# Kernel tuning notes

Measured on AMD Instinct MI355X. Metric: run time of the kernel, lower is better.

## Reference

```python
import jax, jax.numpy as jnp
import numpy as np
from jax import lax

L, H = 16384, 1024
EPS = 1e-5


def _ln(x, w, b):
    m = jnp.mean(x, axis=-1, keepdims=True)
    v = jnp.var(x, axis=-1, keepdims=True)
    return (x - m) * lax.rsqrt(v + EPS) * w + b


def setup_inputs() -> dict:
    key = jax.random.key(0)
    ks = jax.random.split(key, 12)
    s = 0.02
    return {
        "x": jax.random.normal(ks[0], (L, H), dtype=jnp.float32),
        "ln1_w": jnp.ones((H,), jnp.float32),
        "ln1_b": jnp.zeros((H,), jnp.float32),
        "W_in": jax.random.normal(ks[1], (H, H), jnp.float32) * s,
        "b_in": jnp.zeros((H,), jnp.float32),
        "W_gate": jax.random.normal(ks[2], (H, H), jnp.float32) * s,
        "b_gate": jnp.zeros((H,), jnp.float32),
        "W_out": jax.random.normal(ks[3], (H, H), jnp.float32) * s,
        "b_out": jnp.zeros((H,), jnp.float32),
        "state_decay": jnp.zeros((H,), jnp.float32),
        "ln2_w": jnp.ones((H,), jnp.float32),
        "ln2_b": jnp.zeros((H,), jnp.float32),
        "W_ff1": jax.random.normal(ks[4], (H, 2 * H), jnp.float32) * s,
        "b_ff1": jnp.zeros((2 * H,), jnp.float32),
        "W_ff2": jax.random.normal(ks[5], (2 * H, H), jnp.float32) * s,
        "b_ff2": jnp.zeros((H,), jnp.float32),
    }


def reference(x, ln1_w, ln1_b, W_in, b_in, W_gate, b_gate, W_out, b_out,
              state_decay, ln2_w, ln2_b, W_ff1, b_ff1, W_ff2, b_ff2):
    hidden = _ln(x, ln1_w, ln1_b)                       # [L,H]
    u = hidden @ W_in + b_in                            # [L,H]
    gate = jax.nn.sigmoid(hidden @ W_gate + b_gate)     # [L,H]
    decay = jax.nn.sigmoid(state_decay)                 # [H]

    def step(s, u_t):
        s = decay * s + u_t
        return s, s

    z = jnp.zeros((x.shape[1],), x.dtype)
    _, states_f = lax.scan(step, z, u)                  # forward recurrence
    _, states_b = lax.scan(step, z, u, reverse=True)    # backward recurrence
    state_out = 0.5 * (states_f + states_b) * gate

    x = x + state_out @ W_out + b_out
    h = _ln(x, ln2_w, ln2_b)
    x = x + jax.nn.silu(h @ W_ff1 + b_ff1) @ W_ff2 + b_ff2
    return x
```

## Files before the change

kernel.cpp:

```cpp
#include <hip/hip_runtime.h>
#include <hip/hip_bf16.h>
#include <hip/hip_fp16.h>

#define L_SEQ 16384
#define HDIM  1024
#define CH    32
#define NC    (L_SEQ / CH)

typedef _Float16 f16;
typedef _Float16 f16x8 __attribute__((ext_vector_type(8)));
typedef _Float16 f16x4 __attribute__((ext_vector_type(4)));
typedef float    f32x4 __attribute__((ext_vector_type(4)));

#define AS1(p) (const __attribute__((address_space(1))) void*)(p)
#define AS3(p) (__attribute__((address_space(3))) void*)(p)

__global__ __launch_bounds__(256) void wcvt_t(const float* __restrict__ in,
                                              f16* __restrict__ out, int K, int N) {
  __shared__ float tile[32][33];
  int n0 = blockIdx.x * 32, k0 = blockIdx.y * 32;
  int tx = threadIdx.x, ty = threadIdx.y;
#pragma unroll
  for (int i = 0; i < 4; i++) {
    int k = k0 + ty + i * 8;
    tile[ty + i * 8][tx] = in[(size_t)k * N + n0 + tx];
  }
  __syncthreads();
#pragma unroll
  for (int i = 0; i < 4; i++) {
    int n = n0 + ty + i * 8;
    out[(size_t)n * K + k0 + tx] = (f16)tile[tx][ty + i * 8];
  }
}

__global__ __launch_bounds__(256) void ln_k(const float* __restrict__ x,
                                            const float* __restrict__ w,
                                            const float* __restrict__ b,
                                            f16* __restrict__ out,
                                            f16* __restrict__ xcopy) {
  int row = blockIdx.x;
  int t = threadIdx.x;
  const float4* xr = (const float4*)(x + (size_t)row * HDIM);
  float4 v = xr[t];
  float s  = v.x + v.y + v.z + v.w;
  float s2 = v.x * v.x + v.y * v.y + v.z * v.z + v.w * v.w;
#pragma unroll
  for (int off = 32; off > 0; off >>= 1) {
    s  += __shfl_down(s, off);
    s2 += __shfl_down(s2, off);
  }
  __shared__ float red[8];
  int wid = t >> 6, lane = t & 63;
  if (lane == 0) { red[wid] = s; red[4 + wid] = s2; }
  __syncthreads();
  if (t == 0) {
    red[0] = red[0] + red[1] + red[2] + red[3];
    red[4] = red[4] + red[5] + red[6] + red[7];
  }
  __syncthreads();
  float mean = red[0] * (1.0f / HDIM);
  float var  = red[4] * (1.0f / HDIM) - mean * mean;
  float rstd = rsqrtf(var + 1e-5f);
  float4 ww = ((const float4*)w)[t];
  float4 bb = ((const float4*)b)[t];
  f16x4 o;
  o[0] = (f16)((v.x - mean) * rstd * ww.x + bb.x);
  o[1] = (f16)((v.y - mean) * rstd * ww.y + bb.y);
  o[2] = (f16)((v.z - mean) * rstd * ww.z + bb.z);
  o[3] = (f16)((v.w - mean) * rstd * ww.w + bb.w);
  ((f16x4*)(out + (size_t)row * HDIM))[t] = o;
  if (xcopy) {
    f16x4 c;
    c[0] = (f16)v.x; c[1] = (f16)v.y; c[2] = (f16)v.z; c[3] = (f16)v.w;
    ((f16x4*)(xcopy + (size_t)row * HDIM))[t] = c;
  }
}

__global__ __launch_bounds__(128) void ln_k16(const f16* __restrict__ x,
                                              const float* __restrict__ w,
                                              const float* __restrict__ b,
                                              f16* __restrict__ out) {
  int row = blockIdx.x;
  int t = threadIdx.x;
  f16x8 xv = ((const f16x8*)(x + (size_t)row * HDIM))[t];
  float v[8];
  float s = 0.f, s2 = 0.f;
#pragma unroll
  for (int i = 0; i < 8; i++) {
    v[i] = (float)xv[i];
    s += v[i]; s2 += v[i] * v[i];
  }
#pragma unroll
  for (int off = 32; off > 0; off >>= 1) {
    s  += __shfl_down(s, off);
    s2 += __shfl_down(s2, off);
  }
  __shared__ float red[4];
  int wid = t >> 6, lane = t & 63;
  if (lane == 0) { red[wid] = s; red[2 + wid] = s2; }
  __syncthreads();
  float mean = (red[0] + red[1]) * (1.0f / HDIM);
  float var  = (red[2] + red[3]) * (1.0f / HDIM) - mean * mean;
  float rstd = rsqrtf(var + 1e-5f);
  float4 w1 = ((const float4*)w)[2 * t], w2 = ((const float4*)w)[2 * t + 1];
  float4 b1 = ((const float4*)b)[2 * t], b2 = ((const float4*)b)[2 * t + 1];
  float wv[8] = {w1.x, w1.y, w1.z, w1.w, w2.x, w2.y, w2.z, w2.w};
  float bv[8] = {b1.x, b1.y, b1.z, b1.w, b2.x, b2.y, b2.z, b2.w};
  f16x8 o;
#pragma unroll
  for (int i = 0; i < 8; i++) o[i] = (f16)((v[i] - mean) * rstd * wv[i] + bv[i]);
  ((f16x8*)(out + (size_t)row * HDIM))[t] = o;
}

template <int MODE, int RESID, int OUTF16>
__global__ __launch_bounds__(256, 4) void gemm_bt(const f16* __restrict__ A,
                                                  const f16* __restrict__ BT,
                                                  const float* __restrict__ bias,
                                                  const float* __restrict__ bias2,
                                                  const f16* __restrict__ resid,
                                                  void* __restrict__ Cout,
                                                  void* __restrict__ Cout2,
                                                  int M, int N, int K) {
  __shared__ __align__(16) f16 As[2][128 * 32];
  __shared__ __align__(16) f16 Bs[2][128 * 32];
  const int tid  = threadIdx.x;
  const int lane = tid & 63, wid = tid >> 6;
  const int wm = wid >> 1, wn = wid & 1;
  const int quad = lane >> 4, l16 = lane & 15;

  const int nbx = N >> 7, nby = M >> 7;
  const int b = blockIdx.x;
  const int xcd = b & 7;
  const int i = b >> 3;
  const int strips = nby >> 3;
  const int rs = i / nbx, cb = i - rs * nbx;
  const long m0 = (long)(xcd * strips + rs) << 7;
  const long n0 = (long)cb << 7;

  const int srow = wid * 16 + (lane >> 2);
  const int scol = (lane & 3) * 8;
  const f16* gA = A  + (m0 + srow) * K + scol;
  const f16* gB = BT + (n0 + srow) * K + scol;
  const int sdst = wid * 1024;

  f32x4 zero = {0.f, 0.f, 0.f, 0.f};
  f32x4 acc[4][4];
#pragma unroll
  for (int i2 = 0; i2 < 4; i2++)
#pragma unroll
    for (int j = 0; j < 4; j++) acc[i2][j] = zero;

#pragma unroll
  for (int it = 0; it < 2; ++it) {
    __builtin_amdgcn_global_load_lds(AS1(gA + (size_t)(it * 64) * K),
                                     AS3((char*)As[0] + it * 4096 + sdst), 16, 0, 0);
    __builtin_amdgcn_global_load_lds(AS1(gB + (size_t)(it * 64) * K),
                                     AS3((char*)Bs[0] + it * 4096 + sdst), 16, 0, 0);
  }
  __syncthreads();

  const int niter = K >> 5;
  for (int ki = 0; ki < niter; ++ki) {
    const int cur = ki & 1;
    if (ki + 1 < niter) {
      const int nxt = cur ^ 1;
      const int koff = (ki + 1) << 5;
#pragma unroll
      for (int it = 0; it < 2; ++it) {
        __builtin_amdgcn_global_load_lds(AS1(gA + (size_t)(it * 64) * K + koff),
                                         AS3((char*)As[nxt] + it * 4096 + sdst), 16, 0, 0);
        __builtin_amdgcn_global_load_lds(AS1(gB + (size_t)(it * 64) * K + koff),
                                         AS3((char*)Bs[nxt] + it * 4096 + sdst), 16, 0, 0);
      }
    }
    f16x8 af[4], bfr[4];
#pragma unroll
    for (int mi = 0; mi < 4; ++mi)
      af[mi] = *(const f16x8*)(As[cur] + (wm * 64 + mi * 16 + l16) * 32 + quad * 8);
#pragma unroll
    for (int ni = 0; ni < 4; ++ni)
      bfr[ni] = *(const f16x8*)(Bs[cur] + (wn * 64 + ni * 16 + l16) * 32 + quad * 8);
#pragma unroll
    for (int mi = 0; mi < 4; ++mi)
#pragma unroll
      for (int ni = 0; ni < 4; ++ni)
        acc[mi][ni] = __builtin_amdgcn_mfma_f32_16x16x32_f16(bfr[ni], af[mi], acc[mi][ni], 0, 0, 0);
    __syncthreads();
  }

#pragma unroll
  for (int mi = 0; mi < 4; ++mi) {
    const long row = m0 + wm * 64 + mi * 16 + l16;
#pragma unroll
    for (int ni = 0; ni < 4; ++ni) {
      const long col = n0 + wn * 64 + ni * 16 + quad * 4;
      const float* bp;
      if (MODE == 3) bp = (col < HDIM) ? (bias + col) : (bias2 + (col - HDIM));
      else           bp = bias + col;
      f32x4 v = acc[mi][ni] + *(const f32x4*)bp;
      if (MODE == 2) {
#pragma unroll
        for (int r = 0; r < 4; ++r) v[r] = v[r] / (1.f + __expf(-v[r]));
      }
      if (MODE == 3) {
        if (col < HDIM) {
          f16x4 o;
#pragma unroll
          for (int r = 0; r < 4; ++r) o[r] = (f16)v[r];
          *(f16x4*)((f16*)Cout + row * HDIM + col) = o;
        } else {
          f16x4 o;
#pragma unroll
          for (int r = 0; r < 4; ++r) o[r] = (f16)(1.f / (1.f + __expf(-v[r])));
          *(f16x4*)((f16*)Cout2 + row * HDIM + (col - HDIM)) = o;
        }
      } else {
        if (RESID) {
          f16x4 rv = *(const f16x4*)(resid + row * N + col);
#pragma unroll
          for (int r = 0; r < 4; ++r) v[r] += (float)rv[r];
        }
        if (OUTF16) {
          f16x4 o;
#pragma unroll
          for (int r = 0; r < 4; ++r) o[r] = (f16)v[r];
          *(f16x4*)((f16*)Cout + row * N + col) = o;
        } else {
          *(f32x4*)((float*)Cout + row * N + col) = v;
        }
      }
    }
  }
}

__global__ __launch_bounds__(256) void scan_p1(const f16* __restrict__ u,
                                               const float* __restrict__ sdecay,
                                               float* __restrict__ carry_f,
                                               float* __restrict__ carry_b) {
  int tid = blockIdx.x * 256 + threadIdx.x;
  int h = tid & (HDIM - 1);
  int c = tid >> 10;
  float d = 1.f / (1.f + expf(-sdecay[h]));
  const f16* up = u + (size_t)c * CH * HDIM + h;
  float sf = 0.f, sb = 0.f, p = 1.f;
#pragma unroll
  for (int i = 0; i < CH; i++) {
    float uu = (float)up[i * HDIM];
    sf = d * sf + uu;
    sb += p * uu;
    p *= d;
  }
  carry_f[(size_t)c * HDIM + h] = sf;
  carry_b[(size_t)c * HDIM + h] = sb;
}

__global__ __launch_bounds__(256) void scan_p2(const float* __restrict__ sdecay,
                                               const float* __restrict__ carry_f,
                                               const float* __restrict__ carry_b,
                                               float* __restrict__ cin_f,
                                               float* __restrict__ cin_b) {
  int tid = blockIdx.x * 256 + threadIdx.x;
  int h = tid & (HDIM - 1);
  int dir = tid >> 10;
  float d = 1.f / (1.f + expf(-sdecay[h]));
  float dT = powf(d, (float)CH);
  float S = 0.f;
  if (dir == 0) {
#pragma unroll 4
    for (int c = 0; c < NC; c++) {
      cin_f[(size_t)c * HDIM + h] = S;
      S = dT * S + carry_f[(size_t)c * HDIM + h];
    }
  } else {
#pragma unroll 4
    for (int c = NC - 1; c >= 0; c--) {
      cin_b[(size_t)c * HDIM + h] = S;
      S = dT * S + carry_b[(size_t)c * HDIM + h];
    }
  }
}

__global__ __launch_bounds__(256) void scan_p3(const f16* __restrict__ u,
                                               const f16* __restrict__ gate,
                                               const float* __restrict__ sdecay,
                                               const float* __restrict__ cin_f,
                                               const float* __restrict__ cin_b,
                                               f16* __restrict__ state_out) {
  int tid = blockIdx.x * 256 + threadIdx.x;
  int h = tid & (HDIM - 1);
  int c = tid >> 10;
  float d = 1.f / (1.f + expf(-sdecay[h]));
  const f16* up = u    + (size_t)c * CH * HDIM + h;
  const f16* gp = gate + (size_t)c * CH * HDIM + h;
  f16* op = state_out  + (size_t)c * CH * HDIM + h;
  float ur[CH], sf[CH];
#pragma unroll
  for (int i = 0; i < CH; i++) ur[i] = (float)up[i * HDIM];
  float s = cin_f[(size_t)c * HDIM + h];
#pragma unroll
  for (int i = 0; i < CH; i++) { s = d * s + ur[i]; sf[i] = s; }
  s = cin_b[(size_t)c * HDIM + h];
#pragma unroll
  for (int i = CH - 1; i >= 0; i--) {
    s = d * s + ur[i];
    float g = (float)gp[i * HDIM];
    op[i * HDIM] = (f16)(0.5f * (sf[i] + s) * g);
  }
}

extern "C" void kernel_launch(void* const* d_in, const int* in_sizes, int n_in,
                              void* d_out, int out_size, void* d_ws, size_t ws_size,
                              hipStream_t stream) {
  const float* x      = (const float*)d_in[0];
  const float* ln1_w  = (const float*)d_in[1];
  const float* ln1_b  = (const float*)d_in[2];
  const float* W_in   = (const float*)d_in[3];
  const float* b_in   = (const float*)d_in[4];
  const float* W_gate = (const float*)d_in[5];
  const float* b_gate = (const float*)d_in[6];
  const float* W_out  = (const float*)d_in[7];
  const float* b_out  = (const float*)d_in[8];
  const float* sdecay = (const float*)d_in[9];
  const float* ln2_w  = (const float*)d_in[10];
  const float* ln2_b  = (const float*)d_in[11];
  const float* W_ff1  = (const float*)d_in[12];
  const float* b_ff1  = (const float*)d_in[13];
  const float* W_ff2  = (const float*)d_in[14];
  const float* b_ff2  = (const float*)d_in[15];
  float* out = (float*)d_out;

  char* ws = (char*)d_ws;
  const size_t MB32 = 33554432, MB64 = 67108864;
  f16* hidden = (f16*)(ws);
  f16* xh     = (f16*)(ws + MB32);
  f16* u      = (f16*)(ws + 2 * MB32);
  f16* gate   = (f16*)(ws + 3 * MB32);
  f16* x2h    = (f16*)(ws + 4 * MB32);
  f16* ff     = (f16*)(ws + 5 * MB32);
  char* wbase = ws + 5 * MB32 + MB64;
  f16* wt_ug  = (f16*)(wbase);
  f16* wt_out = (f16*)(wbase + 4194304);
  f16* wt_ff1 = (f16*)(wbase + 4194304 + 2097152);
  f16* wt_ff2 = (f16*)(wbase + 2 * 4194304 + 2097152);
  char* cbase = wbase + 3 * 4194304 + 2097152;
  float* carry_f = (float*)(cbase);
  float* carry_b = (float*)(cbase + 2097152);
  float* cin_f   = (float*)(cbase + 2 * 2097152);
  float* cin_b   = (float*)(cbase + 3 * 2097152);
  f16* state_out = hidden;
  f16* h2        = u;

  dim3 tb(32, 8);
  wcvt_t<<<dim3(32, 32), tb, 0, stream>>>(W_in,   wt_ug,                 1024, 1024);
  wcvt_t<<<dim3(32, 32), tb, 0, stream>>>(W_gate, wt_ug + 1024 * 1024,   1024, 1024);
  wcvt_t<<<dim3(32, 32), tb, 0, stream>>>(W_out,  wt_out,                1024, 1024);
  wcvt_t<<<dim3(64, 32), tb, 0, stream>>>(W_ff1,  wt_ff1,                1024, 2048);
  wcvt_t<<<dim3(32, 64), tb, 0, stream>>>(W_ff2,  wt_ff2,                2048, 1024);

  ln_k<<<L_SEQ, 256, 0, stream>>>(x, ln1_w, ln1_b, hidden, xh);

  gemm_bt<3, 0, 1><<<2048, 256, 0, stream>>>(hidden, wt_ug, b_in, b_gate, nullptr,
                                             u, gate, L_SEQ, 2048, 1024);

  scan_p1<<<2048, 256, 0, stream>>>(u, sdecay, carry_f, carry_b);
  scan_p2<<<8, 256, 0, stream>>>(sdecay, carry_f, carry_b, cin_f, cin_b);
  scan_p3<<<2048, 256, 0, stream>>>(u, gate, sdecay, cin_f, cin_b, state_out);

  gemm_bt<0, 1, 1><<<1024, 256, 0, stream>>>(state_out, wt_out, b_out, nullptr, xh,
                                             x2h, nullptr, L_SEQ, 1024, 1024);

  ln_k16<<<L_SEQ, 128, 0, stream>>>(x2h, ln2_w, ln2_b, h2);

  gemm_bt<2, 0, 1><<<2048, 256, 0, stream>>>(h2, wt_ff1, b_ff1, nullptr, nullptr,
                                             ff, nullptr, L_SEQ, 2048, 1024);

  gemm_bt<0, 1, 0><<<1024, 256, 0, stream>>>(ff, wt_ff2, b_ff2, nullptr, x2h,
                                             out, nullptr, L_SEQ, 1024, 2048);
}
```

Measured before the change: 619.4 us.

## Replace 128x128 GEMM with 256x256-tile 8-wave kernel with swizzled LDS and interleaved loads

All four GEMMs now use a 256x256 output tile per 512-thread block, where before they used 128x128 per 256-thread block. The goal is to double operand reuse from LDS and cut global traffic per FLOP. The LDS layout gains an XOR swizzle to avoid bank conflicts. Each K-step is split into two half-phases that issue the next A and B global->LDS loads while the MFMAs run, with explicit barriers, waitcnts and setprio. Larger tiles lower occupancy and halve the number of blocks, which may worsen wave quantization across CUs, and the hand-tuned barrier ordering adds a synchronization risk.

```diff
diff --git a/kernel.cpp b/kernel.cpp
--- a/kernel.cpp
+++ b/kernel.cpp
@@ -113,7 +113,7 @@
 }
 
 template <int MODE, int RESID, int OUTF16>
-__global__ __launch_bounds__(256, 4) void gemm_bt(const f16* __restrict__ A,
+__global__ __launch_bounds__(512, 2) void gemm256(const f16* __restrict__ A,
                                                   const f16* __restrict__ BT,
                                                   const float* __restrict__ bias,
                                                   const float* __restrict__ bias2,
@@ -121,76 +121,116 @@
                                                   void* __restrict__ Cout,
                                                   void* __restrict__ Cout2,
                                                   int M, int N, int K) {
-  __shared__ __align__(16) f16 As[2][128 * 32];
-  __shared__ __align__(16) f16 Bs[2][128 * 32];
+  __shared__ __align__(16) f16 As[2][256 * 32];
+  __shared__ __align__(16) f16 Bs[2][256 * 32];
   const int tid  = threadIdx.x;
-  const int lane = tid & 63, wid = tid >> 6;
-  const int wm = wid >> 1, wn = wid & 1;
+  const int lane = tid & 63;
+  const int wid  = tid >> 6;
+  const int wm = wid >> 2, wn = wid & 3;
   const int quad = lane >> 4, l16 = lane & 15;
-
-  const int nbx = N >> 7, nby = M >> 7;
+  const int xq = (quad ^ ((l16 >> 1) & 3)) << 4;
+
+  const int nbx = N >> 8, nby = M >> 8;
   const int b = blockIdx.x;
   const int xcd = b & 7;
   const int i = b >> 3;
   const int strips = nby >> 3;
   const int rs = i / nbx, cb = i - rs * nbx;
-  const long m0 = (long)(xcd * strips + rs) << 7;
-  const long n0 = (long)cb << 7;
-
-  const int srow = wid * 16 + (lane >> 2);
-  const int scol = (lane & 3) * 8;
-  const f16* gA = A  + (m0 + srow) * K + scol;
-  const f16* gB = BT + (n0 + srow) * K + scol;
-  const int sdst = wid * 1024;
+  const long m0 = (long)(xcd * strips + rs) << 8;
+  const long n0 = (long)cb << 8;
+
+  const int srow = tid >> 2;
+  const int qs = (tid & 3) ^ ((tid >> 3) & 3);
+  const f16* gA = A  + (size_t)(m0 + srow) * K + qs * 8;
+  const f16* gB = BT + (size_t)(n0 + srow) * K + qs * 8;
+  const int sdst = tid * 16;
 
   f32x4 zero = {0.f, 0.f, 0.f, 0.f};
-  f32x4 acc[4][4];
-#pragma unroll
-  for (int i2 = 0; i2 < 4; i2++)
-#pragma unroll
-    for (int j = 0; j < 4; j++) acc[i2][j] = zero;
-
-#pragma unroll
-  for (int it = 0; it < 2; ++it) {
-    __builtin_amdgcn_global_load_lds(AS1(gA + (size_t)(it * 64) * K),
-                                     AS3((char*)As[0] + it * 4096 + sdst), 16, 0, 0);
-    __builtin_amdgcn_global_load_lds(AS1(gB + (size_t)(it * 64) * K),
-                                     AS3((char*)Bs[0] + it * 4096 + sdst), 16, 0, 0);
-  }
-  __syncthreads();
-
-  const int niter = K >> 5;
-  for (int ki = 0; ki < niter; ++ki) {
-    const int cur = ki & 1;
-    if (ki + 1 < niter) {
-      const int nxt = cur ^ 1;
-      const int koff = (ki + 1) << 5;
-#pragma unroll
-      for (int it = 0; it < 2; ++it) {
-        __builtin_amdgcn_global_load_lds(AS1(gA + (size_t)(it * 64) * K + koff),
-                                         AS3((char*)As[nxt] + it * 4096 + sdst), 16, 0, 0);
-        __builtin_amdgcn_global_load_lds(AS1(gB + (size_t)(it * 64) * K + koff),
-                                         AS3((char*)Bs[nxt] + it * 4096 + sdst), 16, 0, 0);
-      }
-    }
-    f16x8 af[4], bfr[4];
+  f32x4 acc[8][4];
+#pragma unroll
+  for (int mi = 0; mi < 8; ++mi)
+#pragma unroll
+    for (int ni = 0; ni < 4; ++ni) acc[mi][ni] = zero;
+
+#pragma unroll
+  for (int h = 0; h < 2; ++h) {
+    __builtin_amdgcn_global_load_lds(AS1(gA + (size_t)h * 128 * K),
+                                     AS3((char*)As[0] + h * 8192 + sdst), 16, 0, 0);
+    __builtin_amdgcn_global_load_lds(AS1(gB + (size_t)h * 128 * K),
+                                     AS3((char*)Bs[0] + h * 8192 + sdst), 16, 0, 0);
+  }
+
+  const int nt = K >> 5;
+  int cur = 0;
+  for (int t = 0; t < nt; ++t) {
+    asm volatile("s_waitcnt vmcnt(0)" ::: "memory");
+    __builtin_amdgcn_sched_barrier(0);
+    __builtin_amdgcn_s_barrier();
+    const f16* Ab = As[cur];
+    const f16* Bb = Bs[cur];
+    const int nxt = cur ^ 1;
+
+    f16x8 af[4], bf[4];
+#pragma unroll
+    for (int mi = 0; mi < 4; ++mi) {
+      const int row = wm * 128 + mi * 16 + l16;
+      af[mi] = *(const f16x8*)((const char*)Ab + row * 64 + xq);
+    }
+#pragma unroll
+    for (int ni = 0; ni < 4; ++ni) {
+      const int row = wn * 64 + ni * 16 + l16;
+      bf[ni] = *(const f16x8*)((const char*)Bb + row * 64 + xq);
+    }
+    if (t + 1 < nt) {
+      const size_t koff = (size_t)(t + 1) * 32;
+#pragma unroll
+      for (int h = 0; h < 2; ++h)
+        __builtin_amdgcn_global_load_lds(AS1(gA + (size_t)h * 128 * K + koff),
+                                         AS3((char*)As[nxt] + h * 8192 + sdst), 16, 0, 0);
+    }
+    __builtin_amdgcn_s_barrier();
+    asm volatile("s_waitcnt lgkmcnt(0)" ::: "memory");
+    __builtin_amdgcn_sched_barrier(0);
+    __builtin_amdgcn_s_setprio(1);
 #pragma unroll
     for (int mi = 0; mi < 4; ++mi)
-      af[mi] = *(const f16x8*)(As[cur] + (wm * 64 + mi * 16 + l16) * 32 + quad * 8);
-#pragma unroll
-    for (int ni = 0; ni < 4; ++ni)
-      bfr[ni] = *(const f16x8*)(Bs[cur] + (wn * 64 + ni * 16 + l16) * 32 + quad * 8);
+#pragma unroll
+      for (int ni = 0; ni < 4; ++ni)
+        acc[mi][ni] = __builtin_amdgcn_mfma_f32_16x16x32_f16(bf[ni], af[mi], acc[mi][ni], 0, 0, 0);
+    __builtin_amdgcn_s_setprio(0);
+    __builtin_amdgcn_sched_barrier(0);
+    __builtin_amdgcn_s_barrier();
+
+    f16x8 af2[4];
+#pragma unroll
+    for (int mi = 0; mi < 4; ++mi) {
+      const int row = wm * 128 + (4 + mi) * 16 + l16;
+      af2[mi] = *(const f16x8*)((const char*)Ab + row * 64 + xq);
+    }
+    if (t + 1 < nt) {
+      const size_t koff = (size_t)(t + 1) * 32;
+#pragma unroll
+      for (int h = 0; h < 2; ++h)
+        __builtin_amdgcn_global_load_lds(AS1(gB + (size_t)h * 128 * K + koff),
+                                         AS3((char*)Bs[nxt] + h * 8192 + sdst), 16, 0, 0);
+    }
+    __builtin_amdgcn_s_barrier();
+    asm volatile("s_waitcnt lgkmcnt(0)" ::: "memory");
+    __builtin_amdgcn_sched_barrier(0);
+    __builtin_amdgcn_s_setprio(1);
 #pragma unroll
     for (int mi = 0; mi < 4; ++mi)
 #pragma unroll
       for (int ni = 0; ni < 4; ++ni)
-        acc[mi][ni] = __builtin_amdgcn_mfma_f32_16x16x32_f16(bfr[ni], af[mi], acc[mi][ni], 0, 0, 0);
-    __syncthreads();
-  }
-
-#pragma unroll
-  for (int mi = 0; mi < 4; ++mi) {
-    const long row = m0 + wm * 64 + mi * 16 + l16;
+        acc[4 + mi][ni] = __builtin_amdgcn_mfma_f32_16x16x32_f16(bf[ni], af2[mi], acc[4 + mi][ni], 0, 0, 0);
+    __builtin_amdgcn_s_setprio(0);
+    __builtin_amdgcn_sched_barrier(0);
+    cur = nxt;
+  }
+
+#pragma unroll
+  for (int mi = 0; mi < 8; ++mi) {
+    const long row = m0 + wm * 128 + mi * 16 + l16;
 #pragma unroll
     for (int ni = 0; ni < 4; ++ni) {
       const long col = n0 + wn * 64 + ni * 16 + quad * 4;
@@ -359,21 +399,21 @@
 
   ln_k<<<L_SEQ, 256, 0, stream>>>(x, ln1_w, ln1_b, hidden, xh);
 
-  gemm_bt<3, 0, 1><<<2048, 256, 0, stream>>>(hidden, wt_ug, b_in, b_gate, nullptr,
-                                             u, gate, L_SEQ, 2048, 1024);
+  gemm256<3, 0, 1><<<512, 512, 0, stream>>>(hidden, wt_ug, b_in, b_gate, nullptr,
+                                            u, gate, L_SEQ, 2048, 1024);
 
   scan_p1<<<2048, 256, 0, stream>>>(u, sdecay, carry_f, carry_b);
   scan_p2<<<8, 256, 0, stream>>>(sdecay, carry_f, carry_b, cin_f, cin_b);
   scan_p3<<<2048, 256, 0, stream>>>(u, gate, sdecay, cin_f, cin_b, state_out);
 
-  gemm_bt<0, 1, 1><<<1024, 256, 0, stream>>>(state_out, wt_out, b_out, nullptr, xh,
-                                             x2h, nullptr, L_SEQ, 1024, 1024);
+  gemm256<0, 1, 1><<<256, 512, 0, stream>>>(state_out, wt_out, b_out, nullptr, xh,
+                                            x2h, nullptr, L_SEQ, 1024, 1024);
 
   ln_k16<<<L_SEQ, 128, 0, stream>>>(x2h, ln2_w, ln2_b, h2);
 
-  gemm_bt<2, 0, 1><<<2048, 256, 0, stream>>>(h2, wt_ff1, b_ff1, nullptr, nullptr,
-                                             ff, nullptr, L_SEQ, 2048, 1024);
-
-  gemm_bt<0, 1, 0><<<1024, 256, 0, stream>>>(ff, wt_ff2, b_ff2, nullptr, x2h,
-                                             out, nullptr, L_SEQ, 1024, 2048);
-}
+  gemm256<2, 0, 1><<<512, 512, 0, stream>>>(h2, wt_ff1, b_ff1, nullptr, nullptr,
+                                            ff, nullptr, L_SEQ, 2048, 1024);
+
+  gemm256<0, 1, 0><<<256, 512, 0, stream>>>(ff, wt_ff2, b_ff2, nullptr, x2h,
+                                            out, nullptr, L_SEQ, 1024, 2048);
+}
```

Result: faster. 592.8 us (-4.3%).
